# Performance work log

Hardware: AMD Instinct MI355X
Metric: run time of the kernel (lower is better)

Reference implementation:

```python
import jax, jax.numpy as jnp
import numpy as np

B, Qn, Kn, QD, KVD, FFN, H = 8, 1024, 2048, 512, 256, 2048, 8


def _layer_norm(x, g, b, eps=1e-5):
    m = jnp.mean(x, axis=-1, keepdims=True)
    v = jnp.mean((x - m) ** 2, axis=-1, keepdims=True)
    return (x - m) * jax.lax.rsqrt(v + eps) * g + b


def _mha(q, k, v, key_padding_mask, num_heads):
    # q,k: [B,S,D], v: [B,K,Dv]; reshape to per-head, scale by sqrt(key head dim)
    b, qn, d = q.shape
    kn = k.shape[1]
    dh = d // num_heads
    q = q.reshape(b, qn, num_heads, dh)
    k = k.reshape(b, kn, num_heads, dh)
    v = v.reshape(b, kn, num_heads, -1)
    attn = jnp.einsum('bqhd,bkhd->bhqk', q, k) / jnp.asarray(np.sqrt(dh), q.dtype)
    attn = jnp.where(key_padding_mask[:, None, None, :], -jnp.inf, attn)
    attn = jax.nn.softmax(attn, axis=-1)
    out = jnp.einsum('bhqk,bkhd->bqhd', attn, v)  # [B,Q,H,dv]
    return out.reshape(b, qn, -1)


def setup_inputs() -> dict:
    key = jax.random.key(0)
    ks = jax.random.split(key, 32)
    s = 0.02
    inp = {
        'queries_data': jax.random.normal(ks[0], (B, Qn, QD), jnp.float32),
        'queries_mask': jnp.zeros((B, Qn), bool),
        'box_pos': jax.random.normal(ks[1], (B, Qn, 4 * KVD), jnp.float32),
        'center_pos': jax.random.normal(ks[2], (B, Qn, 2 * KVD), jnp.float32),
        'kv_data': jax.random.normal(ks[3], (B, Kn, KVD), jnp.float32),
        'kv_mask': jnp.zeros((B, Kn), bool),
        'kv_pos': jax.random.normal(ks[4], (B, Kn, KVD), jnp.float32),
        # params ([in,out] convention)
        'sa_qkv_w': jax.random.normal(ks[5], (QD, 3 * QD), jnp.float32) * s,
        'sa_qkv_b': jnp.zeros((3 * QD,), jnp.float32),
        'sa_pos_w': jax.random.normal(ks[6], (4 * KVD, 2 * QD), jnp.float32) * s,
        'sa_pos_b': jnp.zeros((2 * QD,), jnp.float32),
        'sa_ln_g': jnp.ones((QD,), jnp.float32),
        'sa_ln_b': jnp.zeros((QD,), jnp.float32),
        'ca_q_w': jax.random.normal(ks[7], (QD, QD), jnp.float32) * s,
        'ca_q_b': jnp.zeros((QD,), jnp.float32),
        'ca_kv_w': jax.random.normal(ks[8], (KVD, 2 * QD), jnp.float32) * s,
        'ca_kv_b': jnp.zeros((2 * QD,), jnp.float32),
        'ca_qpos_w': jax.random.normal(ks[9], (2 * KVD, QD), jnp.float32) * s,
        'ca_qpos_b': jnp.zeros((QD,), jnp.float32),
        'ca_kpos_w': jax.random.normal(ks[10], (KVD, QD), jnp.float32) * s,
        'ca_kpos_b': jnp.zeros((QD,), jnp.float32),
        'ca_ln_g': jnp.ones((QD,), jnp.float32),
        'ca_ln_b': jnp.zeros((QD,), jnp.float32),
        'ffn_w1': jax.random.normal(ks[11], (QD, FFN), jnp.float32) * s,
        'ffn_b1': jnp.zeros((FFN,), jnp.float32),
        'ffn_w2': jax.random.normal(ks[12], (FFN, QD), jnp.float32) * s,
        'ffn_b2': jnp.zeros((QD,), jnp.float32),
        'ffn_ln_g': jnp.ones((QD,), jnp.float32),
        'ffn_ln_b': jnp.zeros((QD,), jnp.float32),
    }
    return inp


def reference(queries_data, queries_mask, box_pos, center_pos, kv_data, kv_mask, kv_pos,
              sa_qkv_w, sa_qkv_b, sa_pos_w, sa_pos_b, sa_ln_g, sa_ln_b,
              ca_q_w, ca_q_b, ca_kv_w, ca_kv_b, ca_qpos_w, ca_qpos_b,
              ca_kpos_w, ca_kpos_b, ca_ln_g, ca_ln_b,
              ffn_w1, ffn_b1, ffn_w2, ffn_b2, ffn_ln_g, ffn_ln_b):
    # ---- self-attention (pos added to q,k) ----
    qkv = queries_data @ sa_qkv_w + sa_qkv_b
    q, k, v = jnp.split(qkv, 3, axis=-1)
    q_pos, k_pos = jnp.split(box_pos @ sa_pos_w + sa_pos_b, 2, axis=-1)
    sa_out = _mha(q + q_pos, k + k_pos, v, queries_mask, H)
    sa_out = _layer_norm(queries_data + sa_out, sa_ln_g, sa_ln_b)
    # ---- cross-attention (pos concatenated per head) ----
    q = sa_out @ ca_q_w + ca_q_b
    k, v = jnp.split(kv_data @ ca_kv_w + ca_kv_b, 2, axis=-1)
    q_pos = center_pos @ ca_qpos_w + ca_qpos_b
    k_pos = kv_pos @ ca_kpos_w + ca_kpos_b
    dh = QD // H
    q = jnp.concatenate([q.reshape(B, Qn, H, dh), q_pos.reshape(B, Qn, H, dh)], axis=-1).reshape(B, Qn, -1)
    k = jnp.concatenate([k.reshape(B, Kn, H, dh), k_pos.reshape(B, Kn, H, dh)], axis=-1).reshape(B, Kn, -1)
    ca_out = _mha(q, k, v, kv_mask, H)
    ca_out = _layer_norm(sa_out + ca_out, ca_ln_g, ca_ln_b)
    # ---- FFN ----
    f = jax.nn.relu(ca_out @ ffn_w1 + ffn_b1) @ ffn_w2 + ffn_b2
    return _layer_norm(ca_out + f, ffn_ln_g, ffn_ln_b)
```

## Files before the change

kernel.cpp:

```cpp
#include <hip/hip_runtime.h>

typedef __attribute__((ext_vector_type(4))) float f32x4;
typedef __attribute__((ext_vector_type(8))) short bf16x8;
typedef __attribute__((ext_vector_type(4))) unsigned int u32x4;

static __device__ __forceinline__ short f2bf(float f){
    unsigned int u = __builtin_bit_cast(unsigned int, f);
    unsigned int r = (u + 0x7fffu + ((u >> 16) & 1u)) >> 16;
    return (short)r;
}
static __device__ __forceinline__ void gload_lds16(const void* g, void* l){
    __builtin_amdgcn_global_load_lds((const __attribute__((address_space(1))) void*)g,
                                     (__attribute__((address_space(3))) void*)l, 16, 0, 0);
}
static __device__ __forceinline__ float exp2fast(float x){
    float r; asm("v_exp_f32 %0, %1" : "=v"(r) : "v"(x)); return r;
}
static __device__ __forceinline__ unsigned int packbf(float lo, float hi){
#if __has_builtin(__builtin_amdgcn_perm)
    return __builtin_amdgcn_perm(__builtin_bit_cast(unsigned int, hi),
                                 __builtin_bit_cast(unsigned int, lo), 0x07060302u);
#else
    return (__builtin_bit_cast(unsigned int, hi) & 0xffff0000u) |
           (__builtin_bit_cast(unsigned int, lo) >> 16);
#endif
}
static __device__ __forceinline__ void prio_hi(){
#if defined(__HIP_DEVICE_COMPILE__)
    __builtin_amdgcn_s_setprio(1);
#endif
}
static __device__ __forceinline__ void prio_lo(){
#if defined(__HIP_DEVICE_COMPILE__)
    __builtin_amdgcn_s_setprio(0);
#endif
}
static __device__ __forceinline__ void barrier_raw(){
#if defined(__HIP_DEVICE_COMPILE__)
    __builtin_amdgcn_s_barrier();
#endif
}

static __device__ __forceinline__ void transcast_body(const float* __restrict__ w,
                                                      short* __restrict__ wT,
                                                      int K, int N, int bx, int by, int t){
    int n = bx * 256 + t;
    int k0 = by * 8;
    bf16x8 o;
#pragma unroll
    for (int j = 0; j < 8; j++) o[j] = f2bf(w[(long)(k0 + j) * N + n]);
    *(bf16x8*)(wT + (long)n * K + k0) = o;
}
__global__ __launch_bounds__(256) void prep_weights(
    const float* __restrict__ queries, const float* __restrict__ box,
    const float* __restrict__ ctr, const float* __restrict__ kvd, const float* __restrict__ kvp,
    const unsigned char* __restrict__ qmask, const unsigned char* __restrict__ kmask,
    const float* __restrict__ b_qkv, const float* __restrict__ b_pos,
    short* __restrict__ Xcat, short* __restrict__ ctr_bf,
    short* __restrict__ kvd_bf, short* __restrict__ kvp_bf,
    float* __restrict__ mb_sa, float* __restrict__ mb_ca, float* __restrict__ bcomb,
    const float* __restrict__ w_qkv, const float* __restrict__ w_pos,
    const float* __restrict__ w_caq, const float* __restrict__ w_cakv,
    const float* __restrict__ w_caqp, const float* __restrict__ w_cakp,
    const float* __restrict__ w_f1, const float* __restrict__ w_f2,
    short* __restrict__ wTm_qk, short* __restrict__ wTv,
    short* __restrict__ wT_caq, short* __restrict__ wT_cakv,
    short* __restrict__ wT_caqp, short* __restrict__ wT_cakp,
    short* __restrict__ wT_f1, short* __restrict__ wT_f2)
{
    int bb = blockIdx.x, t = threadIdx.x;
    if (bb < 12288){
        const float* src; short* dst; long i; long stride; int logRow; int colOff;
        if (bb < 2048){ src = queries; dst = Xcat; i = ((long)bb * 256 + t) * 8; logRow = 9;  stride = 1536; colOff = 0; }
        else if (bb < 6144){ src = box; dst = Xcat; i = ((long)(bb - 2048) * 256 + t) * 8; logRow = 10; stride = 1536; colOff = 512; }
        else if (bb < 8192){ src = ctr; dst = ctr_bf; i = ((long)(bb - 6144) * 256 + t) * 8; logRow = 0; stride = 0; colOff = 0; }
        else if (bb < 10240){ src = kvd; dst = kvd_bf; i = ((long)(bb - 8192) * 256 + t) * 8; logRow = 0; stride = 0; colOff = 0; }
        else { src = kvp; dst = kvp_bf; i = ((long)(bb - 10240) * 256 + t) * 8; logRow = 0; stride = 0; colOff = 0; }
        f32x4 a = *(const f32x4*)(src + i);
        f32x4 b = *(const f32x4*)(src + i + 4);
        bf16x8 o;
#pragma unroll
        for (int j = 0; j < 4; j++){ o[j] = f2bf(a[j]); o[4 + j] = f2bf(b[j]); }
        long oi = logRow ? ((i >> logRow) * stride + colOff + (i & ((1L << logRow) - 1))) : i;
        *(bf16x8*)(dst + oi) = o;
        return;
    }
    if (bb < 12320){ int i = (bb - 12288) * 256 + t; mb_sa[i] = qmask[i] ? -1e30f : 0.f; return; }
    if (bb < 12384){ int i = (bb - 12320) * 256 + t; mb_ca[i] = kmask[i] ? -1e30f : 0.f; return; }
    if (bb < 12388){ int i = (bb - 12384) * 256 + t; if (i < 1024) bcomb[i] = b_qkv[i] + b_pos[i]; return; }
    int wb = bb - 12388;
    if (wb < 768){
        int by = wb / 4, bx = wb % 4;
        int n = bx * 256 + t;
        int k0 = by * 8;
        bf16x8 o;
#pragma unroll
        for (int j = 0; j < 8; j++){
            int kk = k0 + j;
            float v = (kk < 512) ? w_qkv[(long)kk * 1536 + n] : w_pos[(long)(kk - 512) * 1024 + n];
            o[j] = f2bf(v);
        }
        *(bf16x8*)(wTm_qk + (long)n * 1536 + k0) = o;
    }
    else if (wb < 896){
        int lb = wb - 768;
        int by = lb / 2, bx = lb % 2;
        int n = bx * 256 + t;
        int k0 = by * 8;
        bf16x8 o;
#pragma unroll
        for (int j = 0; j < 8; j++) o[j] = f2bf(w_qkv[(long)(k0 + j) * 1536 + 1024 + n]);
        *(bf16x8*)(wTv + (long)n * 512 + k0) = o;
    }
    else if (wb < 1024){ int lb = wb - 896;  transcast_body(w_caq,  wT_caq,  512, 512,  lb % 2, lb / 2, t); }
    else if (wb < 1152){ int lb = wb - 1024; transcast_body(w_cakv, wT_cakv, 256, 1024, lb % 4, lb / 4, t); }
    else if (wb < 1280){ int lb = wb - 1152; transcast_body(w_caqp, wT_caqp, 512, 512,  lb % 2, lb / 2, t); }
    else if (wb < 1344){ int lb = wb - 1280; transcast_body(w_cakp, wT_cakp, 256, 512,  lb % 2, lb / 2, t); }
    else if (wb < 1856){ int lb = wb - 1344; transcast_body(w_f1,   wT_f1,   512, 2048, lb % 8, lb / 8, t); }
    else               { int lb = wb - 1856; transcast_body(w_f2,   wT_f2,   2048, 512, lb % 2, lb / 2, t); }
}

struct GD {
    const short* A; const short* Bt; const float* bias;
    short* Cbf; float* Cf; short* Vt;
    long lda;
    int N, K, flags, vtColBase, snShift, vtSN, blkStart, nbx, nblk;
};
struct GD6 { GD g[6]; int n; };

__global__ __launch_bounds__(128, 2) void gemm_multi(GD6 dd)
{
    constexpr int BN = 64, BLOCK = 128;
    constexpr int BUF = (128 + BN) * 32;
    constexpr int EST = BN + 4;
    __shared__ __attribute__((aligned(16))) char smem[3 * BUF * 2];
    float* lC = (float*)smem;
    int bb = blockIdx.x;
    int si = 0;
#pragma unroll
    for (int i = 1; i < 6; i++) if (i < dd.n && bb >= dd.g[i].blkStart) si = i;
    const short* A = dd.g[si].A;
    const short* Bt = dd.g[si].Bt;
    const float* bias = dd.g[si].bias;
    short* Cbf = dd.g[si].Cbf;
    float* Cf = dd.g[si].Cf;
    short* Vt = dd.g[si].Vt;
    long lda = dd.g[si].lda;
    int N = dd.g[si].N, K = dd.g[si].K, flags = dd.g[si].flags;
    int vtColBase = dd.g[si].vtColBase, snShift = dd.g[si].snShift, vtSN = dd.g[si].vtSN;
    int nbx = dd.g[si].nbx, nblk = dd.g[si].nblk;

    int t = threadIdx.x, w = t >> 6, l = t & 63;
    int cl = l & 15, g = l >> 4;
    int flat = bb - dd.g[si].blkStart;
    int q8 = nblk >> 3;
    int swz = (flat & 7) * q8 + (flat >> 3);
    long r0 = (long)(swz / nbx) * 128, c0 = (long)(swz % nbx) * BN;
    int wr = w;
    f32x4 acc[4][4];
#pragma unroll
    for (int mi = 0; mi < 4; mi++)
#pragma unroll
        for (int ni = 0; ni < 4; ni++) acc[mi][ni] = f32x4{0.f, 0.f, 0.f, 0.f};

    auto stage = [&](int d, int k0){
        char* lA = smem + (size_t)d * BUF * 2;
        char* lB = lA + 128 * 32 * 2;
#pragma unroll
        for (int i = 0; i < 4; i++){
            int s = i * BLOCK + t;
            int row = s >> 2, blk = s & 3;
            int sb = blk ^ (row & 3);
            gload_lds16(A + (r0 + row) * lda + k0 + sb * 8, lA + i * (BLOCK * 16) + w * 1024);
        }
#pragma unroll
        for (int i = 0; i < 2; i++){
            int s = i * BLOCK + t;
            int row = s >> 2, blk = s & 3;
            int sb = blk ^ (row & 3);
            gload_lds16(Bt + (c0 + row) * (long)K + k0 + sb * 8, lB + i * (BLOCK * 16) + w * 1024);
        }
    };

    int NK = K / 32;
    stage(0, 0);
    stage(1, 32);
    int bc = 0, bs = 2;
    for (int kt = 0; kt < NK; kt++){
        if (kt + 2 < NK){
            stage(bs, (kt + 2) * 32);
            bs = (bs == 2) ? 0 : bs + 1;
            asm volatile("s_waitcnt vmcnt(12)" ::: "memory");
        } else if (kt + 1 < NK){
            asm volatile("s_waitcnt vmcnt(6)" ::: "memory");
        } else {
            asm volatile("s_waitcnt vmcnt(0)" ::: "memory");
        }
        barrier_raw();
        const short* lA = (const short*)(smem + (size_t)bc * BUF * 2);
        const short* lB = lA + 128 * 32;
        bf16x8 af[4], bfr[4];
#pragma unroll
        for (int mi = 0; mi < 4; mi++){
            int row = wr * 64 + mi * 16 + cl;
            af[mi] = *(const bf16x8*)(lA + row * 32 + (g ^ (row & 3)) * 8);
        }
#pragma unroll
        for (int ni = 0; ni < 4; ni++){
            int row = ni * 16 + cl;
            bfr[ni] = *(const bf16x8*)(lB + row * 32 + (g ^ (row & 3)) * 8);
        }
        prio_hi();
#pragma unroll
        for (int mi = 0; mi < 4; mi++)
#pragma unroll
            for (int ni = 0; ni < 4; ni++)
                acc[mi][ni] = __builtin_amdgcn_mfma_f32_16x16x32_bf16(af[mi], bfr[ni], acc[mi][ni], 0, 0, 0);
        prio_lo();
        asm volatile("s_waitcnt lgkmcnt(0)" ::: "memory");
        barrier_raw();
        bc = (bc == 2) ? 0 : bc + 1;
    }

    bool vtBlock = (flags & 4) && (c0 >= vtColBase);
#pragma unroll
    for (int mi = 0; mi < 4; mi++){
        __syncthreads();
#pragma unroll
        for (int ni = 0; ni < 4; ni++)
#pragma unroll
            for (int rr = 0; rr < 4; rr++)
                lC[(wr * 16 + g * 4 + rr) * EST + ni * 16 + cl] = acc[mi][ni][rr];
        __syncthreads();
        if (vtBlock){
#pragma unroll
            for (int c2 = 0; c2 < 2; c2++){
                int task = t + BLOCK * c2;
                int col = task & 63;
                int wrg = (task >> 6) & 1;
                int ch = task >> 7;
                float bv = bias[c0 + col];
                long qg0 = r0 + wrg * 64 + mi * 16 + ch * 8;
                bf16x8 ob;
#pragma unroll
                for (int j = 0; j < 8; j++)
                    ob[j] = f2bf(lC[(wrg * 16 + ch * 8 + j) * EST + col] + bv);
                long dvg = c0 - vtColBase + col;
                long h = dvg >> 6, dvv = dvg & 63;
                long b = qg0 >> snShift;
                long loc = qg0 & ((1L << snShift) - 1);
                *(bf16x8*)(Vt + ((b * 8 + h) * 64 + dvv) * (long)vtSN + loc) = ob;
            }
        } else {
#pragma unroll
            for (int c2 = 0; c2 < 2; c2++){
                int chunk = t + BLOCK * c2;
                int row = chunk >> 3;
                int coloff = (chunk & 7) * 8;
                long grow = r0 + (row >> 4) * 64 + mi * 16 + (row & 15);
                long gcol = c0 + coloff;
                f32x4 bv0 = *(const f32x4*)(bias + gcol);
                f32x4 bv1 = *(const f32x4*)(bias + gcol + 4);
                float v[8];
#pragma unroll
                for (int j = 0; j < 8; j++){
                    float x = lC[row * EST + coloff + j] + (j < 4 ? bv0[j] : bv1[j - 4]);
                    if (flags & 1) x = fmaxf(x, 0.f);
                    v[j] = x;
                }
                if (Cf){
                    *(f32x4*)(Cf + grow * N + gcol) = f32x4{v[0], v[1], v[2], v[3]};
                    *(f32x4*)(Cf + grow * N + gcol + 4) = f32x4{v[4], v[5], v[6], v[7]};
                } else {
                    bf16x8 ob;
#pragma unroll
                    for (int j = 0; j < 8; j++) ob[j] = f2bf(v[j]);
                    long idx;
                    if (flags & 2){
                        long part = gcol >> 9;
                        long cc = gcol & 511;
                        long b = grow >> 10, qn = grow & 1023;
                        long h = cc >> 6, d = cc & 63;
                        idx = ((part * 64 + b * 8 + h) * 1024 + qn) * 64 + d;
                    } else if (flags & 4){
                        idx = grow * (long)vtColBase + gcol;
                    } else {
                        idx = grow * N + gcol;
                    }
                    *(bf16x8*)(Cbf + idx) = ob;
                }
            }
        }
    }
}

__global__ __launch_bounds__(256) void ln_fuse(const float* __restrict__ a, const float* __restrict__ b,
                                               const float* __restrict__ g, const float* __restrict__ be,
                                               float* __restrict__ outf, short* __restrict__ outb){
    int w = threadIdx.x >> 6, l = threadIdx.x & 63;
    long row = (long)blockIdx.x * 4 + w;
    long base = row * 512 + l * 8;
    f32x4 a0 = *(const f32x4*)(a + base);
    f32x4 a1 = *(const f32x4*)(a + base + 4);
    f32x4 b0 = *(const f32x4*)(b + base);
    f32x4 b1 = *(const f32x4*)(b + base + 4);
    float x[8]; float s = 0.f, s2 = 0.f;
#pragma unroll
    for (int j = 0; j < 4; j++){ x[j] = a0[j] + b0[j]; x[4 + j] = a1[j] + b1[j]; }
#pragma unroll
    for (int j = 0; j < 8; j++){ s += x[j]; s2 += x[j] * x[j]; }
#pragma unroll
    for (int o = 1; o < 64; o <<= 1){ s += __shfl_xor(s, o); s2 += __shfl_xor(s2, o); }
    float mean = s * (1.f / 512.f);
    float rstd = rsqrtf(s2 * (1.f / 512.f) - mean * mean + 1e-5f);
    int c = l * 8;
    f32x4 y0, y1; bf16x8 ob;
#pragma unroll
    for (int j = 0; j < 4; j++){
        float y = (x[j] - mean) * rstd * g[c + j] + be[c + j];
        y0[j] = y; ob[j] = f2bf(y);
    }
#pragma unroll
    for (int j = 0; j < 4; j++){
        float y = (x[4 + j] - mean) * rstd * g[c + 4 + j] + be[c + 4 + j];
        y1[j] = y; ob[4 + j] = f2bf(y);
    }
    *(f32x4*)(outf + base) = y0;
    *(f32x4*)(outf + base + 4) = y1;
    if (outb) *(bf16x8*)(outb + base) = ob;
}

template<int DH, int KN, bool CAT>
__global__ __launch_bounds__(256, 2) void attn_kernel(
    const short* __restrict__ Q1, const short* __restrict__ Q2,
    const short* __restrict__ K1, const short* __restrict__ K2,
    const short* __restrict__ Vt,
    const float* __restrict__ mbias, float* __restrict__ out, float scale2)
{
    constexpr int KT = 64, DV = 64, Qn = 1024, H = 8;
    constexpr int NF = DH / 32;
    constexpr int BPR = DH / 8;
    constexpr int KITER = KT * BPR / 256;
    constexpr int NT = KN / KT;
    __shared__ __attribute__((aligned(16))) short lK[2][KT * DH];
    __shared__ __attribute__((aligned(16))) short lV[2][DV * KT];
    int t = threadIdx.x, w = t >> 6, l = t & 63;
    int cl = l & 15, g = l >> 4;
    int bid = blockIdx.x;
    int bh = (bid & 7) * 8 + (bid >> 6);
    int qb = (bid >> 3) & 7;
    int b = bh >> 3, h = bh & 7;
    int q0 = qb * 128 + w * 32;

    bf16x8 qf[2][NF];
#pragma unroll
    for (int qq = 0; qq < 2; qq++)
#pragma unroll
        for (int f = 0; f < NF; f++){
            if constexpr (CAT){
                const short* src = (f < NF / 2) ? Q1 : Q2;
                qf[qq][f] = *(const bf16x8*)(src + ((long)b * Qn + q0 + qq * 16 + cl) * 512 + h * 64
                                             + (f & (NF / 2 - 1)) * 32 + 8 * g);
            } else {
                qf[qq][f] = *(const bf16x8*)(Q1 + ((long)bh * Qn + q0 + qq * 16 + cl) * DH + f * 32 + 8 * g);
            }
        }

    const short* kp[KITER];
    long kstep[KITER];
#pragma unroll
    for (int i = 0; i < KITER; i++){
        int s_ = i * 256 + t;
        int srow_ = s_ / BPR, blk = s_ % BPR;
        int s32 = srow_ & 31;
        int key = (srow_ & 32) + 8 * ((s32 >> 2) & 3) + 4 * (s32 >> 4) + (s32 & 3);
        int sb = blk ^ (srow_ & 7);
        if constexpr (CAT){
            if (sb < 8){ kp[i] = K1 + ((long)b * KN + key) * 512 + h * 64 + sb * 8; kstep[i] = (long)KT * 512; }
            else       { kp[i] = K2 + ((long)b * KN + key) * 512 + h * 64 + (sb - 8) * 8; kstep[i] = (long)KT * 512; }
        } else {
            kp[i] = K1 + ((long)bh * KN + key) * DH + sb * 8; kstep[i] = (long)KT * DH;
        }
    }
    const short* vp[2];
#pragma unroll
    for (int i = 0; i < 2; i++){
        int s_ = i * 256 + t;
        int srow_ = s_ >> 3, blk = s_ & 7;
        int sb = blk ^ (srow_ & 7);
        vp[i] = Vt + ((long)bh * DV + srow_) * KN + sb * 8;
    }

    auto stage = [&](int d){
#pragma unroll
        for (int i = 0; i < KITER; i++){
            gload_lds16(kp[i], (char*)(&lK[d][0]) + i * 4096 + w * 1024);
            kp[i] += kstep[i];
        }
#pragma unroll
        for (int i = 0; i < 2; i++){
            gload_lds16(vp[i], (char*)(&lV[d][0]) + i * 4096 + w * 1024);
            vp[i] += KT;
        }
    };

    f32x4 st[2][4];
    auto do_qk = [&](int d){
        prio_hi();
#pragma unroll
        for (int o = 0; o < 4; o++){
            int srow_ = o * 16 + cl;
            bf16x8 kf[NF];
#pragma unroll
            for (int f = 0; f < NF; f++){
                int sb = (4 * f + g) ^ (srow_ & 7);
                kf[f] = *(const bf16x8*)(&lK[d][0] + srow_ * DH + sb * 8);
            }
#pragma unroll
            for (int qq = 0; qq < 2; qq++){
                f32x4 acc = f32x4{0.f, 0.f, 0.f, 0.f};
#pragma unroll
                for (int f = 0; f < NF; f++)
                    acc = __builtin_amdgcn_mfma_f32_16x16x32_bf16(kf[f], qf[qq][f], acc, 0, 0, 0);
                st[qq][o] = acc;
            }
        }
        prio_lo();
    };

    const float* mrow = mbias + (long)b * KN;
    bf16x8 vones;
    {
        u32x4 ou; ou[0] = ou[1] = ou[2] = ou[3] = 0x3F803F80u;
        vones = __builtin_bit_cast(bf16x8, ou);
    }
    f32x4 lacc[2];
    f32x4 oacc[2][4];
#pragma unroll
    for (int qq = 0; qq < 2; qq++){
        lacc[qq] = f32x4{0.f, 0.f, 0.f, 0.f};
#pragma unroll
        for (int d = 0; d < 4; d++) oacc[qq][d] = f32x4{0.f, 0.f, 0.f, 0.f};
    }

    f32x4 mb[4];
#pragma unroll
    for (int o = 0; o < 4; o++)
        mb[o] = *(const f32x4*)(mrow + (o >> 1) * 32 + 8 * g + 4 * (o & 1));

    stage(0);
    __syncthreads();
    do_qk(0);

    for (int tt = 0; tt < NT; tt++){
        int cur = tt & 1;
        if (tt + 1 < NT) stage(cur ^ 1);

        bf16x8 pa[2][2];
#pragma unroll
        for (int qq = 0; qq < 2; qq++){
#pragma unroll
            for (int kb = 0; kb < 2; kb++){
                float pA[4], pB[4];
#pragma unroll
                for (int rr = 0; rr < 4; rr++){
                    pA[rr] = exp2fast(fmaf(st[qq][2 * kb][rr], scale2, mb[2 * kb][rr]));
                    pB[rr] = exp2fast(fmaf(st[qq][2 * kb + 1][rr], scale2, mb[2 * kb + 1][rr]));
                }
                u32x4 pk;
                pk[0] = packbf(pA[0], pA[1]);
                pk[1] = packbf(pA[2], pA[3]);
                pk[2] = packbf(pB[0], pB[1]);
                pk[3] = packbf(pB[2], pB[3]);
                pa[qq][kb] = __builtin_bit_cast(bf16x8, pk);
            }
        }
        if (tt + 1 < NT){
#pragma unroll
            for (int o = 0; o < 4; o++)
                mb[o] = *(const f32x4*)(mrow + (tt + 1) * KT + (o >> 1) * 32 + 8 * g + 4 * (o & 1));
        }
        prio_hi();
#pragma unroll
        for (int qq = 0; qq < 2; qq++){
            lacc[qq] = __builtin_amdgcn_mfma_f32_16x16x32_bf16(pa[qq][0], vones, lacc[qq], 0, 0, 0);
            lacc[qq] = __builtin_amdgcn_mfma_f32_16x16x32_bf16(pa[qq][1], vones, lacc[qq], 0, 0, 0);
        }
#pragma unroll
        for (int dvc = 0; dvc < 4; dvc++){
            int vrow = dvc * 16 + cl;
            bf16x8 vf[2];
#pragma unroll
            for (int kb = 0; kb < 2; kb++){
                int sb = (4 * kb + g) ^ (vrow & 7);
                vf[kb] = *(const bf16x8*)(&lV[cur][0] + vrow * KT + sb * 8);
            }
#pragma unroll
            for (int qq = 0; qq < 2; qq++){
                f32x4 o = oacc[qq][dvc];
                o = __builtin_amdgcn_mfma_f32_16x16x32_bf16(pa[qq][0], vf[0], o, 0, 0, 0);
                o = __builtin_amdgcn_mfma_f32_16x16x32_bf16(pa[qq][1], vf[1], o, 0, 0, 0);
                oacc[qq][dvc] = o;
            }
        }
        prio_lo();
        __syncthreads();
        if (tt + 1 < NT) do_qk(cur ^ 1);
    }

#pragma unroll
    for (int qq = 0; qq < 2; qq++){
        float linv[4];
#pragma unroll
        for (int rr = 0; rr < 4; rr++) linv[rr] = 1.f / lacc[qq][rr];
#pragma unroll
        for (int dvc = 0; dvc < 4; dvc++)
#pragma unroll
            for (int rr = 0; rr < 4; rr++){
                int q = q0 + qq * 16 + 4 * g + rr;
                out[(((long)b * Qn + q) * H + h) * DV + dvc * 16 + cl] = oacc[qq][dvc][rr] * linv[rr];
            }
    }
}

extern "C" void kernel_launch(void* const* d_in, const int* in_sizes, int n_in,
                              void* d_out, int out_size, void* d_ws, size_t ws_size,
                              hipStream_t stream)
{
    (void)in_sizes; (void)n_in; (void)out_size; (void)ws_size;
    const int Qn = 1024, Kn = 2048;
    const long MQ = 8L * Qn;
    const long MK = 8L * Kn;

    const float* queries = (const float*)d_in[0];
    const unsigned char* qmask = (const unsigned char*)d_in[1];
    const float* box  = (const float*)d_in[2];
    const float* ctr  = (const float*)d_in[3];
    const float* kvd  = (const float*)d_in[4];
    const unsigned char* kmask = (const unsigned char*)d_in[5];
    const float* kvp  = (const float*)d_in[6];
    const float* w_qkv = (const float*)d_in[7];  const float* b_qkv = (const float*)d_in[8];
    const float* w_pos = (const float*)d_in[9];  const float* b_pos = (const float*)d_in[10];
    const float* g_sa  = (const float*)d_in[11]; const float* be_sa = (const float*)d_in[12];
    const float* w_caq = (const float*)d_in[13]; const float* b_caq = (const float*)d_in[14];
    const float* w_cakv = (const float*)d_in[15]; const float* b_cakv = (const float*)d_in[16];
    const float* w_caqp = (const float*)d_in[17]; const float* b_caqp = (const float*)d_in[18];
    const float* w_cakp = (const float*)d_in[19]; const float* b_cakp = (const float*)d_in[20];
    const float* g_ca  = (const float*)d_in[21]; const float* be_ca = (const float*)d_in[22];
    const float* w_f1  = (const float*)d_in[23]; const float* b_f1 = (const float*)d_in[24];
    const float* w_f2  = (const float*)d_in[25]; const float* b_f2 = (const float*)d_in[26];
    const float* g_f   = (const float*)d_in[27]; const float* be_f = (const float*)d_in[28];

    char* ws = (char*)d_ws;
    size_t off = 0;
    auto alloc = [&](size_t bytes) -> char* {
        char* p = ws + off;
        off += (bytes + 255) & ~(size_t)255;
        return p;
    };
    short* wTm_qk  = (short*)alloc(1024L * 1536 * 2);
    short* wTv     = (short*)alloc(512L * 512 * 2);
    short* wT_caq  = (short*)alloc(512L * 512 * 2);
    short* wT_cakv = (short*)alloc(1024L * 256 * 2);
    short* wT_caqp = (short*)alloc(512L * 512 * 2);
    short* wT_cakp = (short*)alloc(512L * 256 * 2);
    short* wT_f1   = (short*)alloc(2048L * 512 * 2);
    short* wT_f2   = (short*)alloc(512L * 2048 * 2);
    float* bcomb   = (float*)alloc(1024L * 4);
    short* ctr_bf  = (short*)alloc(MQ * 512 * 2);
    short* kvd_bf  = (short*)alloc(MK * 256 * 2);
    short* kvp_bf  = (short*)alloc(MK * 256 * 2);
    short* saln_bf = (short*)alloc(MQ * 512 * 2);
    short* caln_bf = (short*)alloc(MQ * 512 * 2);
    float* sa_ln_f = (float*)alloc(MQ * 512 * 4);
    float* ca_ln_f = (float*)alloc(MQ * 512 * 4);
    float* att_f   = (float*)alloc(MQ * 512 * 4);
    float* f_out   = (float*)alloc(MQ * 512 * 4);
    short* VtSA    = (short*)alloc(64L * 64 * 1024 * 2);
    short* VtCA    = (short*)alloc(64L * 64 * 2048 * 2);
    float* mb_sa   = (float*)alloc(MQ * 4);
    float* mb_ca   = (float*)alloc(MK * 4);
    short* caK     = (short*)alloc(MK * 512 * 2);
    short* cakp_bf = (short*)alloc(MK * 512 * 2);
    short* caq_bf  = (short*)alloc(MQ * 512 * 2);
    short* caqp_bf = (short*)alloc(MQ * 512 * 2);
    char* zone1 = alloc(MQ * 1536 * 2);
    char* zone2 = alloc(MQ * 2048 * 2);

    auto mkgd = [&](const short* A, long lda, const short* Bt, const float* bias,
                    short* Cbf, float* Cf, int M, int N, int K, int flags,
                    short* Vt, int vtColBase, int snShift, int vtSN, int blkStart) -> GD {
        GD d;
        d.A = A; d.Bt = Bt; d.bias = bias; d.Cbf = Cbf; d.Cf = Cf; d.Vt = Vt;
        d.lda = lda; d.N = N; d.K = K; d.flags = flags;
        d.vtColBase = vtColBase; d.snShift = snShift; d.vtSN = vtSN;
        d.blkStart = blkStart; d.nbx = N / 64; d.nblk = (N / 64) * (M / 128);
        return d;
    };
    auto launch_multi = [&](GD6& dd){
        int total = 0;
        for (int i = 0; i < dd.n; i++) total += dd.g[i].nblk;
        for (int i = dd.n; i < 6; i++){ dd.g[i] = dd.g[0]; dd.g[i].blkStart = 0x7fffffff; }
        gemm_multi<<<dim3(total), dim3(128), 0, stream>>>(dd);
    };

    short* Xcat = (short*)zone1;
    prep_weights<<<dim3(14756), dim3(256), 0, stream>>>(
        queries, box, ctr, kvd, kvp, qmask, kmask, b_qkv, b_pos,
        Xcat, ctr_bf, kvd_bf, kvp_bf, mb_sa, mb_ca, bcomb,
        w_qkv, w_pos, w_caq, w_cakv, w_caqp, w_cakp, w_f1, w_f2,
        wTm_qk, wTv, wT_caq, wT_cakv, wT_caqp, wT_cakp, wT_f1, wT_f2);

    short* QKVa = (short*)zone2;
    short* Qa  = QKVa;
    short* Ka  = QKVa + 64L * 1024 * 64;
    {
        GD6 dd; dd.n = 5;
        int s0 = 0;
        dd.g[0] = mkgd(Xcat, 1536, wTm_qk, bcomb, QKVa, nullptr, (int)MQ, 1024, 1536, 2,
                       nullptr, 0, 0, 0, s0);                       s0 += dd.g[0].nblk;
        dd.g[1] = mkgd(kvd_bf, 256, wT_cakv, b_cakv, caK, nullptr, (int)MK, 1024, 256, 4,
                       VtCA, 512, 11, 2048, s0);                    s0 += dd.g[1].nblk;
        dd.g[2] = mkgd(kvp_bf, 256, wT_cakp, b_cakp, cakp_bf, nullptr, (int)MK, 512, 256, 0,
                       nullptr, 0, 0, 0, s0);                       s0 += dd.g[2].nblk;
        dd.g[3] = mkgd(Xcat, 1536, wTv, b_qkv + 1024, nullptr, nullptr, (int)MQ, 512, 512, 4,
                       VtSA, 0, 10, 1024, s0);                      s0 += dd.g[3].nblk;
        dd.g[4] = mkgd(ctr_bf, 512, wT_caqp, b_caqp, caqp_bf, nullptr, (int)MQ, 512, 512, 0,
                       nullptr, 0, 0, 0, s0);
        launch_multi(dd);
    }

    attn_kernel<64, 1024, false><<<dim3(512), dim3(256), 0, stream>>>(
        Qa, nullptr, Ka, nullptr, VtSA, mb_sa, att_f, 0.125f * 1.44269504f);

    ln_fuse<<<dim3((unsigned)(MQ / 4)), dim3(256), 0, stream>>>(queries, att_f, g_sa, be_sa, sa_ln_f, saln_bf);

    {
        GD6 dd; dd.n = 1;
        dd.g[0] = mkgd(saln_bf, 512, wT_caq, b_caq, caq_bf, nullptr, (int)MQ, 512, 512, 0,
                       nullptr, 0, 0, 0, 0);
        launch_multi(dd);
    }

    attn_kernel<128, 2048, true><<<dim3(512), dim3(256), 0, stream>>>(
        caq_bf, caqp_bf, caK, cakp_bf, VtCA, mb_ca, att_f, 0.08838834764831845f * 1.44269504f);

    ln_fuse<<<dim3((unsigned)(MQ / 4)), dim3(256), 0, stream>>>(sa_ln_f, att_f, g_ca, be_ca, ca_ln_f, caln_bf);

    short* mid_bf = (short*)zone2;
    {
        GD6 dd; dd.n = 1;
        dd.g[0] = mkgd(caln_bf, 512, wT_f1, b_f1, mid_bf, nullptr, (int)MQ, 2048, 512, 1,
                       nullptr, 0, 0, 0, 0);
        launch_multi(dd);
    }
    {
        GD6 dd; dd.n = 1;
        dd.g[0] = mkgd(mid_bf, 2048, wT_f2, b_f2, nullptr, f_out, (int)MQ, 512, 2048, 0,
                       nullptr, 0, 0, 0, 0);
        launch_multi(dd);
    }

    ln_fuse<<<dim3((unsigned)(MQ / 4)), dim3(256), 0, stream>>>(ca_ln_f, f_out, g_f, be_f, (float*)d_out, (short*)nullptr);
}
```

Measured before the change: 319.6 us.

## Widen GEMM tile to 128x128 with 4 waves and simple double buffering

The batched GEMM kernel moves from 128x64 tiles with 2 waves to 128x128 tiles with 4 waves arranged 2x2. The pipeline also changes from a 3-stage buffer with manual vmcnt waits and raw barriers to a plain 2-stage double buffer synchronised with __syncthreads. The bigger tile raises reuse of each loaded A and B element and halves the number of blocks. In exchange it gives up prefetch depth, and the full barrier after each k-step may expose load latency.

```diff
diff --git a/kernel.cpp b/kernel.cpp
--- a/kernel.cpp
+++ b/kernel.cpp
@@ -33,11 +33,6 @@
 static __device__ __forceinline__ void prio_lo(){
 #if defined(__HIP_DEVICE_COMPILE__)
     __builtin_amdgcn_s_setprio(0);
-#endif
-}
-static __device__ __forceinline__ void barrier_raw(){
-#if defined(__HIP_DEVICE_COMPILE__)
-    __builtin_amdgcn_s_barrier();
 #endif
 }
 
@@ -128,12 +123,12 @@
 };
 struct GD6 { GD g[6]; int n; };
 
-__global__ __launch_bounds__(128, 2) void gemm_multi(GD6 dd)
+__global__ __launch_bounds__(256, 3) void gemm_multi(GD6 dd)
 {
-    constexpr int BN = 64, BLOCK = 128;
+    constexpr int BN = 128, BLOCK = 256;
     constexpr int BUF = (128 + BN) * 32;
     constexpr int EST = BN + 4;
-    __shared__ __attribute__((aligned(16))) char smem[3 * BUF * 2];
+    __shared__ __attribute__((aligned(16))) char smem[2 * BUF * 2];
     float* lC = (float*)smem;
     int bb = blockIdx.x;
     int si = 0;
@@ -156,7 +151,7 @@
     int q8 = nblk >> 3;
     int swz = (flat & 7) * q8 + (flat >> 3);
     long r0 = (long)(swz / nbx) * 128, c0 = (long)(swz % nbx) * BN;
-    int wr = w;
+    int wr = w >> 1, wc = w & 1;
     f32x4 acc[4][4];
 #pragma unroll
     for (int mi = 0; mi < 4; mi++)
@@ -166,38 +161,29 @@
     auto stage = [&](int d, int k0){
         char* lA = smem + (size_t)d * BUF * 2;
         char* lB = lA + 128 * 32 * 2;
-#pragma unroll
-        for (int i = 0; i < 4; i++){
-            int s = i * BLOCK + t;
-            int row = s >> 2, blk = s & 3;
-            int sb = blk ^ (row & 3);
-            gload_lds16(A + (r0 + row) * lda + k0 + sb * 8, lA + i * (BLOCK * 16) + w * 1024);
-        }
 #pragma unroll
         for (int i = 0; i < 2; i++){
             int s = i * BLOCK + t;
             int row = s >> 2, blk = s & 3;
             int sb = blk ^ (row & 3);
-            gload_lds16(Bt + (c0 + row) * (long)K + k0 + sb * 8, lB + i * (BLOCK * 16) + w * 1024);
+            gload_lds16(A + (r0 + row) * lda + k0 + sb * 8, lA + i * 4096 + w * 1024);
+        }
+#pragma unroll
+        for (int i = 0; i < 2; i++){
+            int s = i * BLOCK + t;
+            int row = s >> 2, blk = s & 3;
+            int sb = blk ^ (row & 3);
+            gload_lds16(Bt + (c0 + row) * (long)K + k0 + sb * 8, lB + i * 4096 + w * 1024);
         }
     };
 
+    stage(0, 0);
+    __syncthreads();
     int NK = K / 32;
-    stage(0, 0);
-    stage(1, 32);
-    int bc = 0, bs = 2;
     for (int kt = 0; kt < NK; kt++){
-        if (kt + 2 < NK){
-            stage(bs, (kt + 2) * 32);
-            bs = (bs == 2) ? 0 : bs + 1;
-            asm volatile("s_waitcnt vmcnt(12)" ::: "memory");
-        } else if (kt + 1 < NK){
-            asm volatile("s_waitcnt vmcnt(6)" ::: "memory");
-        } else {
-            asm volatile("s_waitcnt vmcnt(0)" ::: "memory");
-        }
-        barrier_raw();
-        const short* lA = (const short*)(smem + (size_t)bc * BUF * 2);
+        int cur = kt & 1;
+        if (kt + 1 < NK) stage(cur ^ 1, (kt + 1) * 32);
+        const short* lA = (const short*)(smem + (size_t)cur * BUF * 2);
         const short* lB = lA + 128 * 32;
         bf16x8 af[4], bfr[4];
 #pragma unroll
@@ -207,7 +193,7 @@
         }
 #pragma unroll
         for (int ni = 0; ni < 4; ni++){
-            int row = ni * 16 + cl;
+            int row = wc * 64 + ni * 16 + cl;
             bfr[ni] = *(const bf16x8*)(lB + row * 32 + (g ^ (row & 3)) * 8);
         }
         prio_hi();
@@ -217,9 +203,7 @@
             for (int ni = 0; ni < 4; ni++)
                 acc[mi][ni] = __builtin_amdgcn_mfma_f32_16x16x32_bf16(af[mi], bfr[ni], acc[mi][ni], 0, 0, 0);
         prio_lo();
-        asm volatile("s_waitcnt lgkmcnt(0)" ::: "memory");
-        barrier_raw();
-        bc = (bc == 2) ? 0 : bc + 1;
+        __syncthreads();
     }
 
     bool vtBlock = (flags & 4) && (c0 >= vtColBase);
@@ -230,15 +214,15 @@
         for (int ni = 0; ni < 4; ni++)
 #pragma unroll
             for (int rr = 0; rr < 4; rr++)
-                lC[(wr * 16 + g * 4 + rr) * EST + ni * 16 + cl] = acc[mi][ni][rr];
+                lC[(wr * 16 + g * 4 + rr) * EST + wc * 64 + ni * 16 + cl] = acc[mi][ni][rr];
         __syncthreads();
         if (vtBlock){
 #pragma unroll
             for (int c2 = 0; c2 < 2; c2++){
                 int task = t + BLOCK * c2;
-                int col = task & 63;
-                int wrg = (task >> 6) & 1;
-                int ch = task >> 7;
+                int col = task & (BN - 1);
+                int wrg = (task >> 7) & 1;
+                int ch = task >> 8;
                 float bv = bias[c0 + col];
                 long qg0 = r0 + wrg * 64 + mi * 16 + ch * 8;
                 bf16x8 ob;
@@ -252,11 +236,12 @@
                 *(bf16x8*)(Vt + ((b * 8 + h) * 64 + dvv) * (long)vtSN + loc) = ob;
             }
         } else {
-#pragma unroll
-            for (int c2 = 0; c2 < 2; c2++){
+            constexpr int CPR = BN / 8;
+#pragma unroll
+            for (int c2 = 0; c2 < 32 * CPR / BLOCK; c2++){
                 int chunk = t + BLOCK * c2;
-                int row = chunk >> 3;
-                int coloff = (chunk & 7) * 8;
+                int row = chunk / CPR;
+                int coloff = (chunk % CPR) * 8;
                 long grow = r0 + (row >> 4) * 64 + mi * 16 + (row & 15);
                 long gcol = c0 + coloff;
                 f32x4 bv0 = *(const f32x4*)(bias + gcol);
@@ -594,14 +579,14 @@
         d.A = A; d.Bt = Bt; d.bias = bias; d.Cbf = Cbf; d.Cf = Cf; d.Vt = Vt;
         d.lda = lda; d.N = N; d.K = K; d.flags = flags;
         d.vtColBase = vtColBase; d.snShift = snShift; d.vtSN = vtSN;
-        d.blkStart = blkStart; d.nbx = N / 64; d.nblk = (N / 64) * (M / 128);
+        d.blkStart = blkStart; d.nbx = N / 128; d.nblk = (N / 128) * (M / 128);
         return d;
     };
     auto launch_multi = [&](GD6& dd){
         int total = 0;
         for (int i = 0; i < dd.n; i++) total += dd.g[i].nblk;
         for (int i = dd.n; i < 6; i++){ dd.g[i] = dd.g[0]; dd.g[i].blkStart = 0x7fffffff; }
-        gemm_multi<<<dim3(total), dim3(128), 0, stream>>>(dd);
+        gemm_multi<<<dim3(total), dim3(256), 0, stream>>>(dd);
     };
 
     short* Xcat = (short*)zone1;
```

Measured after the change: 299.3 us. 6.4% less time.
